# Optimization experiments

Measured on AMD Instinct MI355X. Metric: run time of the kernel, lower is better.

## Reference

```python
import jax, jax.numpy as jnp
import numpy as np

B, C, D = 16384, 512, 512
EXT = 2
H = C * EXT
TAU = 1.0          # temperature_train
STEP = 0.05        # langevin_step_size
NOISE = 0.1        # langevin_noise
STEPS = 32         # langevin_steps


def setup_inputs() -> dict:
    key = jax.random.key(0)
    ks = jax.random.split(key, 8)
    s_in = 1.0 / np.sqrt(D)
    s_h = 1.0 / np.sqrt(H)
    return {
        'x': jax.random.normal(ks[0], (B, D), jnp.float32),
        'vanilla_components': jnp.abs(jax.random.normal(ks[1], (C, D), jnp.float32) * 0.1),
        'e_sp': jax.random.normal(ks[2], (C * D,), jnp.float32) * 0.1,
        'W1e': jax.random.normal(ks[3], (D, H), jnp.float32) * s_in,
        'b1e': jnp.zeros((H,), jnp.float32),
        'W2e': jax.random.normal(ks[4], (H, C), jnp.float32) * s_h,
        'b2e': jnp.zeros((C,), jnp.float32),
        'W1r': jax.random.normal(ks[5], (D, H), jnp.float32) * s_in,
        'b1r': jnp.zeros((H,), jnp.float32),
        'W2r': jax.random.normal(ks[6], (H, C), jnp.float32) * s_h,
        'b2r': jnp.zeros((C,), jnp.float32),
    }


def _langevin_gate(e, key):
    """Langevin MCMC on latent u with quadratic energy E(u)=0.5||u||^2 + <e,u>.
    Returns selection probability sigmoid(-u/tau)."""
    def step(u, k):
        grad = u + e  # dE/du
        u = u - STEP * grad + NOISE * jax.random.normal(k, u.shape, u.dtype)
        return u, None
    u, _ = jax.lax.scan(step, jnp.zeros_like(e), jax.random.split(key, STEPS))
    return jax.nn.sigmoid(-u / TAU)


def reference(x, vanilla_components, e_sp, W1e, b1e, W2e, b2e, W1r, b1r, W2r, b2r):
    k1, k2 = jax.random.split(jax.random.key(42))
    # non-negative components
    comps = jnp.abs(vanilla_components)  # [C, D]
    # fixed energy-based sparsity mask over component entries
    p_sp = _langevin_gate(e_sp, k1).reshape(C, D)
    comps = comps * p_sp
    # dynamic per-sample component selection energies via MLP
    h = jax.nn.relu(x @ W1e + b1e)          # [B, H]
    e_dyn = h @ W2e + b2e                   # [B, C]
    gate = _langevin_gate(e_dyn, k2)        # [B, C] soft gates (train mode)
    hr = jax.nn.relu(x @ W1r + b1r)         # [B, H]
    conc = (hr @ W2r + b2r) * gate          # [B, C]
    # aggregate: (concentration * components).sum over components -> [B, D]
    return conc @ comps
```

## Files before the change

### kernel.cpp

```cpp
#include <hip/hip_runtime.h>
#include <hip/hip_bf16.h>
#include <stdint.h>

#define Bn 16384
#define Cn 512
#define Dn 512
#define Hn 1024

#define A32 0.80628851f

typedef __attribute__((ext_vector_type(8))) short bf16x8;
typedef __attribute__((ext_vector_type(4))) float f32x4;
typedef __attribute__((ext_vector_type(2))) float f32x2;

__device__ __forceinline__ ushort f2bf(float f) {
  uint32_t u = __float_as_uint(f);
  return (ushort)((u + 0x7fffu + ((u >> 16) & 1u)) >> 16);
}
__device__ __forceinline__ float b2f(ushort u) {
  return __uint_as_float((uint32_t)u << 16);
}

typedef __attribute__((address_space(3))) uint32_t lds_u32_t;
typedef const __attribute__((address_space(1))) uint32_t glb_u32_t;
__device__ __forceinline__ void gload16(const ushort* g, ushort* l) {
  __builtin_amdgcn_global_load_lds((glb_u32_t*)g, (lds_u32_t*)l, 16, 0, 0);
}

constexpr uint32_t crotl(uint32_t v, int s) {
  return (v << s) | (v >> (32 - s));
}
struct TFOut { uint32_t w0, w1; };
constexpr TFOut ctf(uint32_t k0, uint32_t k1, uint32_t x0, uint32_t x1) {
  const uint32_t ks[3] = {k0, k1, k0 ^ k1 ^ 0x1BD11BDAu};
  const int rot[8] = {13, 15, 26, 6, 17, 29, 16, 24};
  uint32_t a = x0 + k0, b = x1 + k1;
  for (int g = 0; g < 5; ++g) {
    for (int i = 0; i < 4; ++i) {
      int r = rot[(g & 1) * 4 + i];
      a += b; b = crotl(b, r); b ^= a;
    }
    a += ks[(g + 1) % 3];
    b += ks[(g + 2) % 3] + (uint32_t)(g + 1);
  }
  return {a, b};
}
struct KeySched { uint32_t s[64]; uint32_t d[64]; };
constexpr KeySched make_keys() {
  KeySched K{};
  TFOut k1 = ctf(0u, 42u, 0u, 0u);
  TFOut k2 = ctf(0u, 42u, 0u, 1u);
  for (uint32_t t = 0; t < 32; ++t) {
    TFOut ws = ctf(k1.w0, k1.w1, 0u, t);
    K.s[2 * t] = ws.w0; K.s[2 * t + 1] = ws.w1;
    TFOut wd = ctf(k2.w0, k2.w1, 0u, t);
    K.d[2 * t] = wd.w0; K.d[2 * t + 1] = wd.w1;
  }
  return K;
}
__constant__ KeySched KS = make_keys();

__device__ __forceinline__ uint32_t rotl32(uint32_t v, int s) {
  return __builtin_rotateleft32(v, (uint32_t)s);
}
__device__ __forceinline__ uint32_t tf_xor(uint32_t K0, uint32_t K1,
                                           uint32_t KX, uint32_t j) {
  uint32_t a = K0, b = K1 + j;
#define TR(r) { a += b; b = rotl32(b, (r)); b ^= a; }
  TR(13) TR(15) TR(26) TR(6)   a += K1; b += KX + 1u;
  TR(17) TR(29) TR(16) TR(24)  a += KX; b += K0 + 2u;
  TR(13) TR(15) TR(26) TR(6)   a += K0; b += K1 + 3u;
  TR(17) TR(29) TR(16) TR(24)  a += K1; b += KX + 4u;
  TR(13) TR(15) TR(26) TR(6)   a += KX; b += K0 + 5u;
#undef TR
  return a ^ b;
}

__device__ __forceinline__ float bits_to_normal(uint32_t bits) {
  float f = __uint_as_float((bits >> 9) | 0x3f800000u) - 1.0f;
  float x = f * 2.0f - 0x1.fffffep-1f;
  float w = -__logf(1.0f - x * x);
  float p;
  if (w < 5.0f) {
    w -= 2.5f;
    p =            2.81022636e-08f;
    p = fmaf(p, w, 3.43273939e-07f);
    p = fmaf(p, w, -3.5233877e-06f);
    p = fmaf(p, w, -4.39150654e-06f);
    p = fmaf(p, w, 0.00021858087f);
    p = fmaf(p, w, -0.00125372503f);
    p = fmaf(p, w, -0.00417768164f);
    p = fmaf(p, w, 0.246640727f);
    p = fmaf(p, w, 1.50140941f);
  } else {
    w = sqrtf(w) - 3.0f;
    p =            -0.000200214257f;
    p = fmaf(p, w, 0.000100950558f);
    p = fmaf(p, w, 0.00134934322f);
    p = fmaf(p, w, -0.00367342844f);
    p = fmaf(p, w, 0.00573950773f);
    p = fmaf(p, w, -0.0076224613f);
    p = fmaf(p, w, 0.00943887047f);
    p = fmaf(p, w, 1.00167406f);
    p = fmaf(p, w, 2.83297682f);
  }
  return 0x1.6a09e6p+0f * (p * x);
}

__device__ __forceinline__ void z_block(ushort* __restrict__ Z, uint32_t zidx) {
  const uint32_t j0 = (zidx * 256u + threadIdx.x) * 2u;
  const uint32_t j1 = j0 + 1u;
  float z0 = 0.0f, z1 = 0.0f;
#pragma unroll 4
  for (int t = 0; t < 32; ++t) {
    const uint32_t K0 = KS.d[2 * t], K1 = KS.d[2 * t + 1];
    const uint32_t KX = K0 ^ K1 ^ 0x1BD11BDAu;
    uint32_t a0 = K0, b0 = K1 + j0;
    uint32_t a1 = K0, b1 = K1 + j1;
#define R2(r)                                                  \
    a0 += b0; a1 += b1;                                        \
    b0 = rotl32(b0, (r)); b1 = rotl32(b1, (r));                \
    b0 ^= a0; b1 ^= a1;
#define I2(p, q) a0 += (p); a1 += (p); b0 += (q); b1 += (q);
    R2(13) R2(15) R2(26) R2(6)  I2(K1, KX + 1u)
    R2(17) R2(29) R2(16) R2(24) I2(KX, K0 + 2u)
    R2(13) R2(15) R2(26) R2(6)  I2(K0, K1 + 3u)
    R2(17) R2(29) R2(16) R2(24) I2(K1, KX + 4u)
    R2(13) R2(15) R2(26) R2(6)  I2(KX, K0 + 5u)
#undef R2
#undef I2
    uint32_t s0 = a0 ^ b0, s1 = a1 ^ b1;
    float f0 = __uint_as_float((s0 >> 9) | 0x3f800000u) - 1.0f;
    float f1 = __uint_as_float((s1 >> 9) | 0x3f800000u) - 1.0f;
    float x0 = f0 * 2.0f - 0x1.fffffep-1f;
    float x1 = f1 * 2.0f - 0x1.fffffep-1f;
    float w0 = fminf(-__logf(fmaf(-x0, x0, 1.0f)), 5.0f) - 2.5f;
    float w1 = fminf(-__logf(fmaf(-x1, x1, 1.0f)), 5.0f) - 2.5f;
    f32x2 X = {x0, x1}, W = {w0, w1};
    f32x2 P = {2.81022636e-08f, 2.81022636e-08f};
    P = __builtin_elementwise_fma(P, W, (f32x2){3.43273939e-07f, 3.43273939e-07f});
    P = __builtin_elementwise_fma(P, W, (f32x2){-3.5233877e-06f, -3.5233877e-06f});
    P = __builtin_elementwise_fma(P, W, (f32x2){-4.39150654e-06f, -4.39150654e-06f});
    P = __builtin_elementwise_fma(P, W, (f32x2){0.00021858087f, 0.00021858087f});
    P = __builtin_elementwise_fma(P, W, (f32x2){-0.00125372503f, -0.00125372503f});
    P = __builtin_elementwise_fma(P, W, (f32x2){-0.00417768164f, -0.00417768164f});
    P = __builtin_elementwise_fma(P, W, (f32x2){0.246640727f, 0.246640727f});
    P = __builtin_elementwise_fma(P, W, (f32x2){1.50140941f, 1.50140941f});
    f32x2 Q = (P * X) * (f32x2){0.14142135f, 0.14142135f};
    z0 = fmaf(0.95f, z0, Q.x);
    z1 = fmaf(0.95f, z1, Q.y);
  }
  *(ushort2*)(Z + j0) = make_ushort2(f2bf(z0), f2bf(z1));
}

__device__ __forceinline__ void transpose_tile(
    const float* __restrict__ in, ushort* __restrict__ out,
    int N, int K, int tIdx, float T[32][33]) {
  const int ntn = N / 32;
  const int tk = tIdx / ntn, tn = tIdx % ntn;
  const int tx = threadIdx.x & 31, ty = threadIdx.x >> 5;
  const int k0 = tk * 32, n0 = tn * 32;
#pragma unroll
  for (int r = 0; r < 32; r += 8)
    T[ty + r][tx] = in[(size_t)(k0 + ty + r) * N + n0 + tx];
  __syncthreads();
#pragma unroll
  for (int r = 0; r < 32; r += 8)
    out[(size_t)(n0 + ty + r) * K + k0 + tx] = f2bf(T[tx][ty + r]);
}

__device__ __forceinline__ void smask_block(
    const float* __restrict__ vc, const float* __restrict__ e_sp,
    ushort* __restrict__ compsT, int g) {
  uint32_t jj = (uint32_t)g * 256 + threadIdx.x;
  uint32_t c = jj & (Cn - 1), d = jj >> 9;
  uint32_t ridx = c * Dn + d;
  float e = e_sp[ridx];
  float u = 0.0f;
#pragma unroll 4
  for (int t = 0; t < 32; ++t) {
    const uint32_t K0 = KS.s[2 * t], K1 = KS.s[2 * t + 1];
    uint32_t s = tf_xor(K0, K1, K0 ^ K1 ^ 0x1BD11BDAu, ridx);
    float n = bits_to_normal(s);
    u = (u - 0.05f * (u + e)) + 0.1f * n;
  }
  float gt = 1.0f / (1.0f + __expf(u));
  compsT[jj] = f2bf(fabsf(vc[ridx]) * gt);
}

__global__ __launch_bounds__(256) void k_prep_z(
    const float* __restrict__ x, ushort* __restrict__ x_bf,
    const float* __restrict__ W1e, ushort* __restrict__ W1eT,
    const float* __restrict__ W2e, ushort* __restrict__ W2eT,
    const float* __restrict__ W1r, ushort* __restrict__ W1rT,
    const float* __restrict__ W2r, ushort* __restrict__ W2rT,
    const float* __restrict__ vc, const float* __restrict__ e_sp,
    ushort* __restrict__ compsT, ushort* __restrict__ Zd) {
  __shared__ float T[32][33];
  const int pos = blockIdx.x;
  if ((pos % 5) == 4) {
    z_block(Zd, (uint32_t)(pos / 5));
    return;
  }
  const int p = (pos / 5) * 4 + (pos % 5);
  if (p < 8192) {
    int i = (p * 256 + threadIdx.x) * 4;
    float4 v = *(const float4*)(x + i);
    *(ushort4*)(x_bf + i) =
        make_ushort4(f2bf(v.x), f2bf(v.y), f2bf(v.z), f2bf(v.w));
  } else if (p < 8704) {
    transpose_tile(W1e, W1eT, Hn, Dn, p - 8192, T);
  } else if (p < 9216) {
    transpose_tile(W2e, W2eT, Cn, Hn, p - 8704, T);
  } else if (p < 9728) {
    transpose_tile(W1r, W1rT, Hn, Dn, p - 9216, T);
  } else if (p < 10240) {
    transpose_tile(W2r, W2rT, Cn, Hn, p - 9728, T);
  } else {
    smask_block(vc, e_sp, compsT, p - 10240);
  }
}

__device__ __forceinline__ void stage4(
    const ushort* ga0, const ushort* ga1,
    const ushort* gb0, const ushort* gb1,
    int k, ushort* As, ushort* Bs, int wo) {
  gload16(ga0 + k, As + wo);
  gload16(ga1 + k, As + 2048 + wo);
  gload16(gb0 + k, Bs + wo);
  gload16(gb1 + k, Bs + 2048 + wo);
}

__device__ __forceinline__ void mfma16(
    const ushort* Ac, const ushort* Bc,
    int wm, int wn, int l15, int rc, f32x4 acc[4][4]) {
  bf16x8 af[4], bfr[4];
#pragma unroll
  for (int i = 0; i < 4; ++i) {
    af[i]  = *(const bf16x8*)&Ac[(wm + i * 16 + l15) * 32 + rc];
    bfr[i] = *(const bf16x8*)&Bc[(wn + i * 16 + l15) * 32 + rc];
  }
#pragma unroll
  for (int i = 0; i < 4; ++i)
#pragma unroll
    for (int j = 0; j < 4; ++j)
      acc[i][j] = __builtin_amdgcn_mfma_f32_16x16x32_bf16(af[i], bfr[j],
                                                          acc[i][j], 0, 0, 0);
}

__device__ __forceinline__ void gemm_core(
    const ushort* __restrict__ A, const ushort* __restrict__ WT,
    int m0, int n0, int LD, int K,
    ushort* __restrict__ As0, ushort* __restrict__ Bs0,
    ushort* __restrict__ As1, ushort* __restrict__ Bs1,
    f32x4 acc[4][4]) {
  const int t = threadIdx.x;
  const int wave = t >> 6, lane = t & 63;
  const int row = t >> 2;
  const int col8 = ((t & 3) << 3) ^ (((t >> 3) & 3) << 3);
  const int wm = (wave >> 1) << 6, wn = (wave & 1) << 6;
  const int quad = lane >> 4, l15 = lane & 15;
  const int rc = (quad << 3) ^ (((l15 >> 1) & 3) << 3);
  const int wo = wave * 512;

  const ushort* ga0 = A  + (size_t)(m0 + row) * LD + col8;
  const ushort* ga1 = A  + (size_t)(m0 + 64 + row) * LD + col8;
  const ushort* gb0 = WT + (size_t)(n0 + row) * LD + col8;
  const ushort* gb1 = WT + (size_t)(n0 + 64 + row) * LD + col8;

  stage4(ga0, ga1, gb0, gb1, 0, As0, Bs0, wo);

  for (int k0 = 0; k0 < K; k0 += 64) {
    stage4(ga0, ga1, gb0, gb1, k0 + 32, As1, Bs1, wo);
    asm volatile("s_waitcnt vmcnt(4)" ::: "memory");
    __builtin_amdgcn_sched_barrier(0);
    __builtin_amdgcn_s_barrier();
    mfma16(As0, Bs0, wm, wn, l15, rc, acc);
    __builtin_amdgcn_s_barrier();
    if (k0 + 64 < K) {
      stage4(ga0, ga1, gb0, gb1, k0 + 64, As0, Bs0, wo);
      asm volatile("s_waitcnt vmcnt(4)" ::: "memory");
    } else {
      asm volatile("s_waitcnt vmcnt(0)" ::: "memory");
    }
    __builtin_amdgcn_sched_barrier(0);
    __builtin_amdgcn_s_barrier();
    mfma16(As1, Bs1, wm, wn, l15, rc, acc);
    __builtin_amdgcn_s_barrier();
  }
}

__device__ __forceinline__ void gemm_tile_bf(
    const ushort* __restrict__ A, const ushort* __restrict__ WT,
    const float* __restrict__ bias, ushort* __restrict__ Out, int g,
    ushort* As0, ushort* Bs0, ushort* As1, ushort* Bs1) {
  const int n0 = (g & 7) * 128, m0 = (g >> 3) * 128;
  const int t = threadIdx.x;
  const int wave = t >> 6, lane = t & 63;
  const int wm = (wave >> 1) << 6, wn = (wave & 1) << 6;
  const int quad = lane >> 4, l15 = lane & 15;
  f32x4 acc[4][4] = {};
  gemm_core(A, WT, m0, n0, Dn, Dn, As0, Bs0, As1, Bs1, acc);
#pragma unroll
  for (int i = 0; i < 4; ++i)
#pragma unroll
    for (int j = 0; j < 4; ++j) {
      const int col = n0 + wn + j * 16 + l15;
      const float bv = bias[col];
#pragma unroll
      for (int r = 0; r < 4; ++r) {
        const int row = m0 + wm + i * 16 + quad * 4 + r;
        Out[(size_t)row * Hn + col] = f2bf(fmaxf(acc[i][j][r] + bv, 0.0f));
      }
    }
}

__global__ __launch_bounds__(256) void k_g13_z(
    const ushort* __restrict__ x_bf,
    const ushort* __restrict__ W1eT, const float* __restrict__ b1e,
    ushort* __restrict__ h,
    const ushort* __restrict__ W1rT, const float* __restrict__ b1r,
    ushort* __restrict__ hr, ushort* __restrict__ Zd) {
  __shared__ ushort As0[4096];
  __shared__ ushort Bs0[4096];
  __shared__ ushort As1[4096];
  __shared__ ushort Bs1[4096];
  const int pos = blockIdx.x;
  if (pos % 3) {
    z_block(Zd, 2816u + (uint32_t)(pos / 3) * 2u + (uint32_t)(pos % 3) - 1u);
    return;
  }
  const int gg = pos / 3;
  const int g = gg >> 1;
  if (gg & 1)
    gemm_tile_bf(x_bf, W1rT, b1r, hr, g, As0, Bs0, As1, Bs1);
  else
    gemm_tile_bf(x_bf, W1eT, b1e, h, g, As0, Bs0, As1, Bs1);
}

__device__ __forceinline__ void gemm_tile_f32out(
    const ushort* __restrict__ A, const ushort* __restrict__ WT,
    const float* __restrict__ bias, float* __restrict__ Out,
    int m0, int n0, ushort* As0, ushort* Bs0, ushort* As1, ushort* Bs1) {
  const int t = threadIdx.x;
  const int wave = t >> 6, lane = t & 63;
  const int wm = (wave >> 1) << 6, wn = (wave & 1) << 6;
  const int quad = lane >> 4, l15 = lane & 15;
  f32x4 acc[4][4] = {};
  gemm_core(A, WT, m0, n0, Hn, Hn, As0, Bs0, As1, Bs1, acc);
#pragma unroll
  for (int i = 0; i < 4; ++i)
#pragma unroll
    for (int j = 0; j < 4; ++j) {
      const int col = n0 + wn + j * 16 + l15;
      const float bv = bias[col];
#pragma unroll
      for (int r = 0; r < 4; ++r) {
        const int row = m0 + wm + i * 16 + quad * 4 + r;
        Out[(size_t)row * Cn + col] = acc[i][j][r] + bv;
      }
    }
}

__global__ __launch_bounds__(256) void k_e_z(
    const ushort* __restrict__ h, const ushort* __restrict__ W2eT,
    const float* __restrict__ b2e, float* __restrict__ e_out,
    ushort* __restrict__ Zd) {
  __shared__ ushort As0[4096];
  __shared__ ushort Bs0[4096];
  __shared__ ushort As1[4096];
  __shared__ ushort Bs1[4096];
  const int pos = blockIdx.x;
  if ((pos % 10) == 0) {
    const int tg = pos / 10;
    gemm_tile_f32out(h, W2eT, b2e, e_out, (tg >> 2) * 128, (tg & 3) * 128,
                     As0, Bs0, As1, Bs1);
  } else {
    z_block(Zd, 6912u + (uint32_t)(pos / 10) * 9u + (uint32_t)(pos % 10) - 1u);
  }
}

__global__ __launch_bounds__(256) void k_r_z(
    const ushort* __restrict__ hr, const ushort* __restrict__ W2rT,
    const float* __restrict__ b2r, float* __restrict__ cr_out,
    ushort* __restrict__ Zd) {
  __shared__ ushort As0[4096];
  __shared__ ushort Bs0[4096];
  __shared__ ushort As1[4096];
  __shared__ ushort Bs1[4096];
  const int pos = blockIdx.x;
  if (pos >= 5120) {
    z_block(Zd, 16128u + (uint32_t)(pos - 5120));
    return;
  }
  if ((pos % 10) == 0) {
    const int tg = pos / 10;
    gemm_tile_f32out(hr, W2rT, b2r, cr_out, (tg >> 2) * 128, (tg & 3) * 128,
                     As0, Bs0, As1, Bs1);
  } else {
    z_block(Zd, 11520u + (uint32_t)(pos / 10) * 9u + (uint32_t)(pos % 10) - 1u);
  }
}

__global__ __launch_bounds__(256) void k_gate(
    const float* __restrict__ e, const float* __restrict__ cr,
    ushort* __restrict__ Z) {
  const size_t i = ((size_t)blockIdx.x * 256u + threadIdx.x) * 8u;
  uint4 zv = *(const uint4*)(Z + i);
  ushort zs[8];
  *(uint4*)zs = zv;
  float ee[8], cc[8];
  *(float4*)(ee)     = *(const float4*)(e + i);
  *(float4*)(ee + 4) = *(const float4*)(e + i + 4);
  *(float4*)(cc)     = *(const float4*)(cr + i);
  *(float4*)(cc + 4) = *(const float4*)(cr + i + 4);
  ushort os[8];
#pragma unroll
  for (int k = 0; k < 8; ++k) {
    float z = b2f(zs[k]);
    float g = 1.0f / (1.0f + __expf(z - A32 * ee[k]));
    os[k] = f2bf(cc[k] * g);
  }
  *(uint4*)(Z + i) = *(uint4*)os;
}

__global__ __launch_bounds__(256) void k_gemm_out(
    const ushort* __restrict__ A, const ushort* __restrict__ WT,
    float* __restrict__ Out) {
  __shared__ ushort As0[4096];
  __shared__ ushort Bs0[4096];
  __shared__ ushort As1[4096];
  __shared__ ushort Bs1[4096];
  const int t = threadIdx.x;
  const int m0 = blockIdx.y * 128, n0 = blockIdx.x * 128;
  const int wave = t >> 6, lane = t & 63;
  const int wm = (wave >> 1) << 6, wn = (wave & 1) << 6;
  const int quad = lane >> 4, l15 = lane & 15;
  f32x4 acc[4][4] = {};
  gemm_core(A, WT, m0, n0, Cn, Cn, As0, Bs0, As1, Bs1, acc);
#pragma unroll
  for (int i = 0; i < 4; ++i)
#pragma unroll
    for (int j = 0; j < 4; ++j) {
      const int col = n0 + wn + j * 16 + l15;
#pragma unroll
      for (int r = 0; r < 4; ++r) {
        const int row = m0 + wm + i * 16 + quad * 4 + r;
        Out[(size_t)row * Dn + col] = acc[i][j][r];
      }
    }
}

extern "C" void kernel_launch(void* const* d_in, const int* in_sizes, int n_in,
                              void* d_out, int out_size, void* d_ws, size_t ws_size,
                              hipStream_t stream) {
  const float* x    = (const float*)d_in[0];
  const float* vc   = (const float*)d_in[1];
  const float* e_sp = (const float*)d_in[2];
  const float* W1e  = (const float*)d_in[3];
  const float* b1e  = (const float*)d_in[4];
  const float* W2e  = (const float*)d_in[5];
  const float* b2e  = (const float*)d_in[6];
  const float* W1r  = (const float*)d_in[7];
  const float* b1r  = (const float*)d_in[8];
  const float* W2r  = (const float*)d_in[9];
  const float* b2r  = (const float*)d_in[10];
  float* out = (float*)d_out;

  char* ws = (char*)d_ws;
  ushort* W1eT   = (ushort*)(ws + (1u << 12));
  ushort* W2eT   = (ushort*)(ws + (1u << 12) + (1u << 20));
  ushort* W1rT   = (ushort*)(ws + (1u << 12) + (2u << 20));
  ushort* W2rT   = (ushort*)(ws + (1u << 12) + (3u << 20));
  ushort* compsT = (ushort*)(ws + (1u << 12) + (4u << 20));
  ushort* Zdyn   = (ushort*)(ws + (8u << 20));
  ushort* h_bf   = (ushort*)(ws + (24u << 20));
  ushort* hr_bf  = (ushort*)(ws + (56u << 20));
  float*  cr_f32 = (float*)(ws + (24u << 20));
  ushort* x_bf   = (ushort*)d_out;
  float*  e_f32  = (float*)d_out;

  k_prep_z<<<14080, 256, 0, stream>>>(x, x_bf, W1e, W1eT, W2e, W2eT,
                                      W1r, W1rT, W2r, W2rT, vc, e_sp, compsT,
                                      Zdyn);
  k_g13_z<<<6144, 256, 0, stream>>>(x_bf, W1eT, b1e, h_bf, W1rT, b1r, hr_bf,
                                    Zdyn);
  k_e_z<<<5120, 256, 0, stream>>>(h_bf, W2eT, b2e, e_f32, Zdyn);
  k_r_z<<<5376, 256, 0, stream>>>(hr_bf, W2rT, b2r, cr_f32, Zdyn);
  k_gate<<<4096, 256, 0, stream>>>(e_f32, cr_f32, Zdyn);
  k_gemm_out<<<dim3(Dn / 128, Bn / 128), 256, 0, stream>>>(Zdyn, compsT, out);
}
```

Measured before the change: 777.5 us.

## Shrink MLP GEMM tiles to 64x64 with single-buffer LDS and higher occupancy

Replaces the 128x128 double-buffered GEMM core used by the three MLP GEMMs with a 64x64 tile, single-buffered LDS loop that synchronizes every 32-wide K step. Launch bounds request 8 blocks per CU, and grid interleaving with the Z-noise generation blocks is remapped to match the new tile counts. The output GEMM keeps the original pipelined 128x128 core, now inlined. Smaller tiles raise occupancy and interleaving granularity, but they lower data reuse per loaded byte and lose the load/compute overlap of the double buffer.

Result: slower. 844.6 us (+8.6%).

```diff
diff --git a/kernel.cpp b/kernel.cpp
--- a/kernel.cpp
+++ b/kernel.cpp
@@ -188,7 +188,7 @@
   compsT[jj] = f2bf(fabsf(vc[ridx]) * gt);
 }
 
-__global__ __launch_bounds__(256) void k_prep_z(
+__global__ __launch_bounds__(256, 8) void k_prep_z(
     const float* __restrict__ x, ushort* __restrict__ x_bf,
     const float* __restrict__ W1e, ushort* __restrict__ W1eT,
     const float* __restrict__ W2e, ushort* __restrict__ W2eT,
@@ -221,184 +221,143 @@
   }
 }
 
-__device__ __forceinline__ void stage4(
-    const ushort* ga0, const ushort* ga1,
-    const ushort* gb0, const ushort* gb1,
-    int k, ushort* As, ushort* Bs, int wo) {
-  gload16(ga0 + k, As + wo);
-  gload16(ga1 + k, As + 2048 + wo);
-  gload16(gb0 + k, Bs + wo);
-  gload16(gb1 + k, Bs + 2048 + wo);
-}
-
-__device__ __forceinline__ void mfma16(
-    const ushort* Ac, const ushort* Bc,
-    int wm, int wn, int l15, int rc, f32x4 acc[4][4]) {
-  bf16x8 af[4], bfr[4];
-#pragma unroll
-  for (int i = 0; i < 4; ++i) {
-    af[i]  = *(const bf16x8*)&Ac[(wm + i * 16 + l15) * 32 + rc];
-    bfr[i] = *(const bf16x8*)&Bc[(wn + i * 16 + l15) * 32 + rc];
-  }
-#pragma unroll
-  for (int i = 0; i < 4; ++i)
-#pragma unroll
-    for (int j = 0; j < 4; ++j)
-      acc[i][j] = __builtin_amdgcn_mfma_f32_16x16x32_bf16(af[i], bfr[j],
-                                                          acc[i][j], 0, 0, 0);
-}
-
-__device__ __forceinline__ void gemm_core(
+__device__ __forceinline__ void gemm_core64(
     const ushort* __restrict__ A, const ushort* __restrict__ WT,
     int m0, int n0, int LD, int K,
-    ushort* __restrict__ As0, ushort* __restrict__ Bs0,
-    ushort* __restrict__ As1, ushort* __restrict__ Bs1,
-    f32x4 acc[4][4]) {
+    ushort* __restrict__ AsL, ushort* __restrict__ BsL,
+    f32x4 acc[2][2]) {
   const int t = threadIdx.x;
   const int wave = t >> 6, lane = t & 63;
   const int row = t >> 2;
   const int col8 = ((t & 3) << 3) ^ (((t >> 3) & 3) << 3);
-  const int wm = (wave >> 1) << 6, wn = (wave & 1) << 6;
+  const int wr = (wave >> 1) << 5, wc = (wave & 1) << 5;
   const int quad = lane >> 4, l15 = lane & 15;
   const int rc = (quad << 3) ^ (((l15 >> 1) & 3) << 3);
-  const int wo = wave * 512;
-
-  const ushort* ga0 = A  + (size_t)(m0 + row) * LD + col8;
-  const ushort* ga1 = A  + (size_t)(m0 + 64 + row) * LD + col8;
-  const ushort* gb0 = WT + (size_t)(n0 + row) * LD + col8;
-  const ushort* gb1 = WT + (size_t)(n0 + 64 + row) * LD + col8;
-
-  stage4(ga0, ga1, gb0, gb1, 0, As0, Bs0, wo);
-
-  for (int k0 = 0; k0 < K; k0 += 64) {
-    stage4(ga0, ga1, gb0, gb1, k0 + 32, As1, Bs1, wo);
-    asm volatile("s_waitcnt vmcnt(4)" ::: "memory");
-    __builtin_amdgcn_sched_barrier(0);
-    __builtin_amdgcn_s_barrier();
-    mfma16(As0, Bs0, wm, wn, l15, rc, acc);
-    __builtin_amdgcn_s_barrier();
-    if (k0 + 64 < K) {
-      stage4(ga0, ga1, gb0, gb1, k0 + 64, As0, Bs0, wo);
-      asm volatile("s_waitcnt vmcnt(4)" ::: "memory");
-    } else {
-      asm volatile("s_waitcnt vmcnt(0)" ::: "memory");
+
+  const ushort* ga = A  + (size_t)(m0 + row) * LD + col8;
+  const ushort* gb = WT + (size_t)(n0 + row) * LD + col8;
+  ushort* la = AsL + wave * 512;
+  ushort* lb = BsL + wave * 512;
+
+  for (int k0 = 0; k0 < K; k0 += 32) {
+    gload16(ga + k0, la);
+    gload16(gb + k0, lb);
+    __syncthreads();
+    bf16x8 af[2], bfr[2];
+#pragma unroll
+    for (int i = 0; i < 2; ++i) {
+      af[i]  = *(const bf16x8*)&AsL[(wr + i * 16 + l15) * 32 + rc];
+      bfr[i] = *(const bf16x8*)&BsL[(wc + i * 16 + l15) * 32 + rc];
     }
-    __builtin_amdgcn_sched_barrier(0);
-    __builtin_amdgcn_s_barrier();
-    mfma16(As1, Bs1, wm, wn, l15, rc, acc);
-    __builtin_amdgcn_s_barrier();
-  }
-}
-
-__device__ __forceinline__ void gemm_tile_bf(
+#pragma unroll
+    for (int i = 0; i < 2; ++i)
+#pragma unroll
+      for (int j = 0; j < 2; ++j)
+        acc[i][j] = __builtin_amdgcn_mfma_f32_16x16x32_bf16(af[i], bfr[j],
+                                                            acc[i][j], 0, 0, 0);
+    __syncthreads();
+  }
+}
+
+__device__ __forceinline__ void gemm_tile_bf64(
     const ushort* __restrict__ A, const ushort* __restrict__ WT,
-    const float* __restrict__ bias, ushort* __restrict__ Out, int g,
-    ushort* As0, ushort* Bs0, ushort* As1, ushort* Bs1) {
-  const int n0 = (g & 7) * 128, m0 = (g >> 3) * 128;
+    const float* __restrict__ bias, ushort* __restrict__ Out,
+    int m0, int n0, ushort* AsL, ushort* BsL) {
   const int t = threadIdx.x;
   const int wave = t >> 6, lane = t & 63;
-  const int wm = (wave >> 1) << 6, wn = (wave & 1) << 6;
+  const int wr = (wave >> 1) << 5, wc = (wave & 1) << 5;
   const int quad = lane >> 4, l15 = lane & 15;
-  f32x4 acc[4][4] = {};
-  gemm_core(A, WT, m0, n0, Dn, Dn, As0, Bs0, As1, Bs1, acc);
-#pragma unroll
-  for (int i = 0; i < 4; ++i)
-#pragma unroll
-    for (int j = 0; j < 4; ++j) {
-      const int col = n0 + wn + j * 16 + l15;
+  f32x4 acc[2][2] = {};
+  gemm_core64(A, WT, m0, n0, Dn, Dn, AsL, BsL, acc);
+#pragma unroll
+  for (int i = 0; i < 2; ++i)
+#pragma unroll
+    for (int j = 0; j < 2; ++j) {
+      const int col = n0 + wc + j * 16 + l15;
       const float bv = bias[col];
 #pragma unroll
       for (int r = 0; r < 4; ++r) {
-        const int row = m0 + wm + i * 16 + quad * 4 + r;
+        const int row = m0 + wr + i * 16 + quad * 4 + r;
         Out[(size_t)row * Hn + col] = f2bf(fmaxf(acc[i][j][r] + bv, 0.0f));
       }
     }
 }
 
-__global__ __launch_bounds__(256) void k_g13_z(
+__global__ __launch_bounds__(256, 8) void k_g13_z(
     const ushort* __restrict__ x_bf,
     const ushort* __restrict__ W1eT, const float* __restrict__ b1e,
     ushort* __restrict__ h,
     const ushort* __restrict__ W1rT, const float* __restrict__ b1r,
     ushort* __restrict__ hr, ushort* __restrict__ Zd) {
-  __shared__ ushort As0[4096];
-  __shared__ ushort Bs0[4096];
-  __shared__ ushort As1[4096];
-  __shared__ ushort Bs1[4096];
+  __shared__ ushort AsL[2048];
+  __shared__ ushort BsL[2048];
   const int pos = blockIdx.x;
-  if (pos % 3) {
-    z_block(Zd, 2816u + (uint32_t)(pos / 3) * 2u + (uint32_t)(pos % 3) - 1u);
+  if ((pos % 3) == 2) {
+    z_block(Zd, 2816u + (uint32_t)(pos / 3));
     return;
   }
-  const int gg = pos / 3;
+  const int gg = (pos / 3) * 2 + (pos % 3);
   const int g = gg >> 1;
+  const int m0 = (g >> 4) * 64, n0 = (g & 15) * 64;
   if (gg & 1)
-    gemm_tile_bf(x_bf, W1rT, b1r, hr, g, As0, Bs0, As1, Bs1);
+    gemm_tile_bf64(x_bf, W1rT, b1r, hr, m0, n0, AsL, BsL);
   else
-    gemm_tile_bf(x_bf, W1eT, b1e, h, g, As0, Bs0, As1, Bs1);
-}
-
-__device__ __forceinline__ void gemm_tile_f32out(
+    gemm_tile_bf64(x_bf, W1eT, b1e, h, m0, n0, AsL, BsL);
+}
+
+__device__ __forceinline__ void gemm_tile_f32out64(
     const ushort* __restrict__ A, const ushort* __restrict__ WT,
     const float* __restrict__ bias, float* __restrict__ Out,
-    int m0, int n0, ushort* As0, ushort* Bs0, ushort* As1, ushort* Bs1) {
+    int m0, int n0, ushort* AsL, ushort* BsL) {
   const int t = threadIdx.x;
   const int wave = t >> 6, lane = t & 63;
-  const int wm = (wave >> 1) << 6, wn = (wave & 1) << 6;
+  const int wr = (wave >> 1) << 5, wc = (wave & 1) << 5;
   const int quad = lane >> 4, l15 = lane & 15;
-  f32x4 acc[4][4] = {};
-  gemm_core(A, WT, m0, n0, Hn, Hn, As0, Bs0, As1, Bs1, acc);
-#pragma unroll
-  for (int i = 0; i < 4; ++i)
-#pragma unroll
-    for (int j = 0; j < 4; ++j) {
-      const int col = n0 + wn + j * 16 + l15;
+  f32x4 acc[2][2] = {};
+  gemm_core64(A, WT, m0, n0, Hn, Hn, AsL, BsL, acc);
+#pragma unroll
+  for (int i = 0; i < 2; ++i)
+#pragma unroll
+    for (int j = 0; j < 2; ++j) {
+      const int col = n0 + wc + j * 16 + l15;
       const float bv = bias[col];
 #pragma unroll
       for (int r = 0; r < 4; ++r) {
-        const int row = m0 + wm + i * 16 + quad * 4 + r;
+        const int row = m0 + wr + i * 16 + quad * 4 + r;
         Out[(size_t)row * Cn + col] = acc[i][j][r] + bv;
       }
     }
 }
 
-__global__ __launch_bounds__(256) void k_e_z(
+__global__ __launch_bounds__(256, 8) void k_e_z(
     const ushort* __restrict__ h, const ushort* __restrict__ W2eT,
     const float* __restrict__ b2e, float* __restrict__ e_out,
     ushort* __restrict__ Zd) {
-  __shared__ ushort As0[4096];
-  __shared__ ushort Bs0[4096];
-  __shared__ ushort As1[4096];
-  __shared__ ushort Bs1[4096];
+  __shared__ ushort AsL[2048];
+  __shared__ ushort BsL[2048];
   const int pos = blockIdx.x;
-  if ((pos % 10) == 0) {
-    const int tg = pos / 10;
-    gemm_tile_f32out(h, W2eT, b2e, e_out, (tg >> 2) * 128, (tg & 3) * 128,
-                     As0, Bs0, As1, Bs1);
+  if ((pos % 13) < 4) {
+    const int tg = (pos / 13) * 4 + (pos % 13);
+    gemm_tile_f32out64(h, W2eT, b2e, e_out, (tg >> 3) * 64, (tg & 7) * 64,
+                       AsL, BsL);
   } else {
-    z_block(Zd, 6912u + (uint32_t)(pos / 10) * 9u + (uint32_t)(pos % 10) - 1u);
-  }
-}
-
-__global__ __launch_bounds__(256) void k_r_z(
+    z_block(Zd, 6912u + (uint32_t)((pos / 13) * 9 + (pos % 13) - 4));
+  }
+}
+
+__global__ __launch_bounds__(256, 8) void k_r_z(
     const ushort* __restrict__ hr, const ushort* __restrict__ W2rT,
     const float* __restrict__ b2r, float* __restrict__ cr_out,
     ushort* __restrict__ Zd) {
-  __shared__ ushort As0[4096];
-  __shared__ ushort Bs0[4096];
-  __shared__ ushort As1[4096];
-  __shared__ ushort Bs1[4096];
+  __shared__ ushort AsL[2048];
+  __shared__ ushort BsL[2048];
   const int pos = blockIdx.x;
-  if (pos >= 5120) {
-    z_block(Zd, 16128u + (uint32_t)(pos - 5120));
-    return;
-  }
-  if ((pos % 10) == 0) {
-    const int tg = pos / 10;
-    gemm_tile_f32out(hr, W2rT, b2r, cr_out, (tg >> 2) * 128, (tg & 3) * 128,
-                     As0, Bs0, As1, Bs1);
+  if ((pos % 27) < 8) {
+    const int tg = (pos / 27) * 8 + (pos % 27);
+    gemm_tile_f32out64(hr, W2rT, b2r, cr_out, (tg >> 3) * 64, (tg & 7) * 64,
+                       AsL, BsL);
   } else {
-    z_block(Zd, 11520u + (uint32_t)(pos / 10) * 9u + (uint32_t)(pos % 10) - 1u);
+    z_block(Zd, 11520u + (uint32_t)((pos / 27) * 19 + (pos % 27) - 8));
   }
 }
 
@@ -424,6 +383,33 @@
   *(uint4*)(Z + i) = *(uint4*)os;
 }
 
+__device__ __forceinline__ void stage4(
+    const ushort* ga0, const ushort* ga1,
+    const ushort* gb0, const ushort* gb1,
+    int k, ushort* As, ushort* Bs, int wo) {
+  gload16(ga0 + k, As + wo);
+  gload16(ga1 + k, As + 2048 + wo);
+  gload16(gb0 + k, Bs + wo);
+  gload16(gb1 + k, Bs + 2048 + wo);
+}
+
+__device__ __forceinline__ void mfma16(
+    const ushort* Ac, const ushort* Bc,
+    int wm, int wn, int l15, int rc, f32x4 acc[4][4]) {
+  bf16x8 af[4], bfr[4];
+#pragma unroll
+  for (int i = 0; i < 4; ++i) {
+    af[i]  = *(const bf16x8*)&Ac[(wm + i * 16 + l15) * 32 + rc];
+    bfr[i] = *(const bf16x8*)&Bc[(wn + i * 16 + l15) * 32 + rc];
+  }
+#pragma unroll
+  for (int i = 0; i < 4; ++i)
+#pragma unroll
+    for (int j = 0; j < 4; ++j)
+      acc[i][j] = __builtin_amdgcn_mfma_f32_16x16x32_bf16(af[i], bfr[j],
+                                                          acc[i][j], 0, 0, 0);
+}
+
 __global__ __launch_bounds__(256) void k_gemm_out(
     const ushort* __restrict__ A, const ushort* __restrict__ WT,
     float* __restrict__ Out) {
@@ -434,10 +420,38 @@
   const int t = threadIdx.x;
   const int m0 = blockIdx.y * 128, n0 = blockIdx.x * 128;
   const int wave = t >> 6, lane = t & 63;
+  const int row = t >> 2;
+  const int col8 = ((t & 3) << 3) ^ (((t >> 3) & 3) << 3);
   const int wm = (wave >> 1) << 6, wn = (wave & 1) << 6;
   const int quad = lane >> 4, l15 = lane & 15;
+  const int rc = (quad << 3) ^ (((l15 >> 1) & 3) << 3);
+  const int wo = wave * 512;
+
+  const ushort* ga0 = A  + (size_t)(m0 + row) * Cn + col8;
+  const ushort* ga1 = A  + (size_t)(m0 + 64 + row) * Cn + col8;
+  const ushort* gb0 = WT + (size_t)(n0 + row) * Cn + col8;
+  const ushort* gb1 = WT + (size_t)(n0 + 64 + row) * Cn + col8;
+
   f32x4 acc[4][4] = {};
-  gemm_core(A, WT, m0, n0, Cn, Cn, As0, Bs0, As1, Bs1, acc);
+  stage4(ga0, ga1, gb0, gb1, 0, As0, Bs0, wo);
+  for (int k0 = 0; k0 < Cn; k0 += 64) {
+    stage4(ga0, ga1, gb0, gb1, k0 + 32, As1, Bs1, wo);
+    asm volatile("s_waitcnt vmcnt(4)" ::: "memory");
+    __builtin_amdgcn_sched_barrier(0);
+    __builtin_amdgcn_s_barrier();
+    mfma16(As0, Bs0, wm, wn, l15, rc, acc);
+    __builtin_amdgcn_s_barrier();
+    if (k0 + 64 < Cn) {
+      stage4(ga0, ga1, gb0, gb1, k0 + 64, As0, Bs0, wo);
+      asm volatile("s_waitcnt vmcnt(4)" ::: "memory");
+    } else {
+      asm volatile("s_waitcnt vmcnt(0)" ::: "memory");
+    }
+    __builtin_amdgcn_sched_barrier(0);
+    __builtin_amdgcn_s_barrier();
+    mfma16(As1, Bs1, wm, wn, l15, rc, acc);
+    __builtin_amdgcn_s_barrier();
+  }
 #pragma unroll
   for (int i = 0; i < 4; ++i)
 #pragma unroll
@@ -445,8 +459,8 @@
       const int col = n0 + wn + j * 16 + l15;
 #pragma unroll
       for (int r = 0; r < 4; ++r) {
-        const int row = m0 + wm + i * 16 + quad * 4 + r;
-        Out[(size_t)row * Dn + col] = acc[i][j][r];
+        const int row2 = m0 + wm + i * 16 + quad * 4 + r;
+        Out[(size_t)row2 * Dn + col] = acc[i][j][r];
       }
     }
 }
@@ -483,10 +497,10 @@
   k_prep_z<<<14080, 256, 0, stream>>>(x, x_bf, W1e, W1eT, W2e, W2eT,
                                       W1r, W1rT, W2r, W2rT, vc, e_sp, compsT,
                                       Zdyn);
-  k_g13_z<<<6144, 256, 0, stream>>>(x_bf, W1eT, b1e, h_bf, W1rT, b1r, hr_bf,
-                                    Zdyn);
-  k_e_z<<<5120, 256, 0, stream>>>(h_bf, W2eT, b2e, e_f32, Zdyn);
-  k_r_z<<<5376, 256, 0, stream>>>(hr_bf, W2rT, b2r, cr_f32, Zdyn);
+  k_g13_z<<<12288, 256, 0, stream>>>(x_bf, W1eT, b1e, h_bf, W1rT, b1r, hr_bf,
+                                     Zdyn);
+  k_e_z<<<6656, 256, 0, stream>>>(h_bf, W2eT, b2e, e_f32, Zdyn);
+  k_r_z<<<6912, 256, 0, stream>>>(hr_bf, W2rT, b2r, cr_f32, Zdyn);
   k_gate<<<4096, 256, 0, stream>>>(e_f32, cr_f32, Zdyn);
   k_gemm_out<<<dim3(Dn / 128, Bn / 128), 256, 0, stream>>>(Zdyn, compsT, out);
 }
```

## Fuse Langevin noise generation into first-layer GEMM k-loop with 512-thread blocks

Applied to the files above, without the earlier changes.

Replaces the interleaved grid of separate GEMM blocks and RNG-only blocks with 512-thread blocks that each compute a 128x128 GEMM tile and, inside every k-iteration, also run two Langevin noise steps for their own slice of Z. The aim is to hide the VALU-heavy Threefry/erfinv work under MFMA and memory latency inside the same wave. The GEMM becomes single-buffered with a 32-wide k-step and two syncthreads per iteration, which loses the previous double-buffered prefetch. It also raises register pressure under launch_bounds(512,6).

Measured after the change: 771.3 us. No clear change (-0.8%).

```diff
diff --git a/kernel.cpp b/kernel.cpp
--- a/kernel.cpp
+++ b/kernel.cpp
@@ -107,49 +107,52 @@
   return 0x1.6a09e6p+0f * (p * x);
 }
 
+__device__ __forceinline__ void z_step(int t, uint32_t j0, uint32_t j1,
+                                       float& z0, float& z1) {
+  const uint32_t K0 = KS.d[2 * t], K1 = KS.d[2 * t + 1];
+  const uint32_t KX = K0 ^ K1 ^ 0x1BD11BDAu;
+  uint32_t a0 = K0, b0 = K1 + j0;
+  uint32_t a1 = K0, b1 = K1 + j1;
+#define R2(r)                                                  \
+  a0 += b0; a1 += b1;                                          \
+  b0 = rotl32(b0, (r)); b1 = rotl32(b1, (r));                  \
+  b0 ^= a0; b1 ^= a1;
+#define I2(p, q) a0 += (p); a1 += (p); b0 += (q); b1 += (q);
+  R2(13) R2(15) R2(26) R2(6)  I2(K1, KX + 1u)
+  R2(17) R2(29) R2(16) R2(24) I2(KX, K0 + 2u)
+  R2(13) R2(15) R2(26) R2(6)  I2(K0, K1 + 3u)
+  R2(17) R2(29) R2(16) R2(24) I2(K1, KX + 4u)
+  R2(13) R2(15) R2(26) R2(6)  I2(KX, K0 + 5u)
+#undef R2
+#undef I2
+  uint32_t s0 = a0 ^ b0, s1 = a1 ^ b1;
+  float f0 = __uint_as_float((s0 >> 9) | 0x3f800000u) - 1.0f;
+  float f1 = __uint_as_float((s1 >> 9) | 0x3f800000u) - 1.0f;
+  float x0 = f0 * 2.0f - 0x1.fffffep-1f;
+  float x1 = f1 * 2.0f - 0x1.fffffep-1f;
+  float w0 = fminf(-__logf(fmaf(-x0, x0, 1.0f)), 5.0f) - 2.5f;
+  float w1 = fminf(-__logf(fmaf(-x1, x1, 1.0f)), 5.0f) - 2.5f;
+  f32x2 X = {x0, x1}, W = {w0, w1};
+  f32x2 P = {2.81022636e-08f, 2.81022636e-08f};
+  P = __builtin_elementwise_fma(P, W, (f32x2){3.43273939e-07f, 3.43273939e-07f});
+  P = __builtin_elementwise_fma(P, W, (f32x2){-3.5233877e-06f, -3.5233877e-06f});
+  P = __builtin_elementwise_fma(P, W, (f32x2){-4.39150654e-06f, -4.39150654e-06f});
+  P = __builtin_elementwise_fma(P, W, (f32x2){0.00021858087f, 0.00021858087f});
+  P = __builtin_elementwise_fma(P, W, (f32x2){-0.00125372503f, -0.00125372503f});
+  P = __builtin_elementwise_fma(P, W, (f32x2){-0.00417768164f, -0.00417768164f});
+  P = __builtin_elementwise_fma(P, W, (f32x2){0.246640727f, 0.246640727f});
+  P = __builtin_elementwise_fma(P, W, (f32x2){1.50140941f, 1.50140941f});
+  f32x2 Q = (P * X) * (f32x2){0.14142135f, 0.14142135f};
+  z0 = fmaf(0.95f, z0, Q.x);
+  z1 = fmaf(0.95f, z1, Q.y);
+}
+
 __device__ __forceinline__ void z_block(ushort* __restrict__ Z, uint32_t zidx) {
   const uint32_t j0 = (zidx * 256u + threadIdx.x) * 2u;
   const uint32_t j1 = j0 + 1u;
   float z0 = 0.0f, z1 = 0.0f;
 #pragma unroll 4
-  for (int t = 0; t < 32; ++t) {
-    const uint32_t K0 = KS.d[2 * t], K1 = KS.d[2 * t + 1];
-    const uint32_t KX = K0 ^ K1 ^ 0x1BD11BDAu;
-    uint32_t a0 = K0, b0 = K1 + j0;
-    uint32_t a1 = K0, b1 = K1 + j1;
-#define R2(r)                                                  \
-    a0 += b0; a1 += b1;                                        \
-    b0 = rotl32(b0, (r)); b1 = rotl32(b1, (r));                \
-    b0 ^= a0; b1 ^= a1;
-#define I2(p, q) a0 += (p); a1 += (p); b0 += (q); b1 += (q);
-    R2(13) R2(15) R2(26) R2(6)  I2(K1, KX + 1u)
-    R2(17) R2(29) R2(16) R2(24) I2(KX, K0 + 2u)
-    R2(13) R2(15) R2(26) R2(6)  I2(K0, K1 + 3u)
-    R2(17) R2(29) R2(16) R2(24) I2(K1, KX + 4u)
-    R2(13) R2(15) R2(26) R2(6)  I2(KX, K0 + 5u)
-#undef R2
-#undef I2
-    uint32_t s0 = a0 ^ b0, s1 = a1 ^ b1;
-    float f0 = __uint_as_float((s0 >> 9) | 0x3f800000u) - 1.0f;
-    float f1 = __uint_as_float((s1 >> 9) | 0x3f800000u) - 1.0f;
-    float x0 = f0 * 2.0f - 0x1.fffffep-1f;
-    float x1 = f1 * 2.0f - 0x1.fffffep-1f;
-    float w0 = fminf(-__logf(fmaf(-x0, x0, 1.0f)), 5.0f) - 2.5f;
-    float w1 = fminf(-__logf(fmaf(-x1, x1, 1.0f)), 5.0f) - 2.5f;
-    f32x2 X = {x0, x1}, W = {w0, w1};
-    f32x2 P = {2.81022636e-08f, 2.81022636e-08f};
-    P = __builtin_elementwise_fma(P, W, (f32x2){3.43273939e-07f, 3.43273939e-07f});
-    P = __builtin_elementwise_fma(P, W, (f32x2){-3.5233877e-06f, -3.5233877e-06f});
-    P = __builtin_elementwise_fma(P, W, (f32x2){-4.39150654e-06f, -4.39150654e-06f});
-    P = __builtin_elementwise_fma(P, W, (f32x2){0.00021858087f, 0.00021858087f});
-    P = __builtin_elementwise_fma(P, W, (f32x2){-0.00125372503f, -0.00125372503f});
-    P = __builtin_elementwise_fma(P, W, (f32x2){-0.00417768164f, -0.00417768164f});
-    P = __builtin_elementwise_fma(P, W, (f32x2){0.246640727f, 0.246640727f});
-    P = __builtin_elementwise_fma(P, W, (f32x2){1.50140941f, 1.50140941f});
-    f32x2 Q = (P * X) * (f32x2){0.14142135f, 0.14142135f};
-    z0 = fmaf(0.95f, z0, Q.x);
-    z1 = fmaf(0.95f, z1, Q.y);
-  }
+  for (int t = 0; t < 32; ++t) z_step(t, j0, j1, z0, z1);
   *(ushort2*)(Z + j0) = make_ushort2(f2bf(z0), f2bf(z1));
 }
 
@@ -219,6 +222,87 @@
   } else {
     smask_block(vc, e_sp, compsT, p - 10240);
   }
+}
+
+template <int KIT, int ZS>
+__device__ __forceinline__ void gemm_z_fused(
+    const ushort* __restrict__ A, const ushort* __restrict__ WT,
+    int m0, int n0, int LD,
+    ushort* __restrict__ AsL, ushort* __restrict__ BsL,
+    f32x4 acc[4][2], uint32_t j0, uint32_t j1, float& z0, float& z1) {
+  const int t = threadIdx.x;
+  const int wave = t >> 6, lane = t & 63;
+  const int row = t >> 2;
+  const int col8 = ((t & 3) << 3) ^ (((t >> 3) & 3) << 3);
+  const int wm = (wave >> 2) << 6, wn = (wave & 3) << 5;
+  const int l15 = lane & 15, quad = lane >> 4;
+  const int rc = (quad << 3) ^ (((l15 >> 1) & 3) << 3);
+
+  const ushort* ga = A  + (size_t)(m0 + row) * LD + col8;
+  const ushort* gb = WT + (size_t)(n0 + row) * LD + col8;
+  ushort* la = AsL + wave * 512;
+  ushort* lb = BsL + wave * 512;
+
+  for (int it = 0; it < KIT; ++it) {
+    gload16(ga + it * 32, la);
+    gload16(gb + it * 32, lb);
+    __syncthreads();
+    bf16x8 af[4], bfr[2];
+#pragma unroll
+    for (int i = 0; i < 4; ++i)
+      af[i] = *(const bf16x8*)&AsL[(wm + i * 16 + l15) * 32 + rc];
+#pragma unroll
+    for (int j = 0; j < 2; ++j)
+      bfr[j] = *(const bf16x8*)&BsL[(wn + j * 16 + l15) * 32 + rc];
+#pragma unroll
+    for (int i = 0; i < 4; ++i)
+#pragma unroll
+      for (int j = 0; j < 2; ++j)
+        acc[i][j] = __builtin_amdgcn_mfma_f32_16x16x32_bf16(af[i], bfr[j],
+                                                            acc[i][j], 0, 0, 0);
+#pragma unroll
+    for (int s = 0; s < ZS; ++s)
+      z_step(it * ZS + s, j0, j1, z0, z1);
+    __syncthreads();
+  }
+}
+
+__global__ __launch_bounds__(512, 6) void k_g13_z(
+    const ushort* __restrict__ x_bf,
+    const ushort* __restrict__ W1eT, const float* __restrict__ b1e,
+    ushort* __restrict__ h,
+    const ushort* __restrict__ W1rT, const float* __restrict__ b1r,
+    ushort* __restrict__ hr, ushort* __restrict__ Zd) {
+  __shared__ ushort AsL[4096];
+  __shared__ ushort BsL[4096];
+  const int pos = blockIdx.x;
+  const uint32_t j0 = 1441792u + (uint32_t)pos * 1024u +
+                      (uint32_t)threadIdx.x * 2u;
+  const uint32_t j1 = j0 + 1u;
+  float z0 = 0.0f, z1 = 0.0f;
+  const int tg = pos >> 1;
+  const int m0 = (tg >> 3) * 128, n0 = (tg & 7) * 128;
+  const ushort* WTp = (pos & 1) ? W1rT : W1eT;
+  const float*  bp  = (pos & 1) ? b1r  : b1e;
+  ushort*       Op  = (pos & 1) ? hr   : h;
+  f32x4 acc[4][2] = {};
+  gemm_z_fused<16, 2>(x_bf, WTp, m0, n0, Dn, AsL, BsL, acc, j0, j1, z0, z1);
+  *(ushort2*)(Zd + j0) = make_ushort2(f2bf(z0), f2bf(z1));
+  const int wave = threadIdx.x >> 6, lane = threadIdx.x & 63;
+  const int wm = (wave >> 2) << 6, wn = (wave & 3) << 5;
+  const int quad = lane >> 4, l15 = lane & 15;
+#pragma unroll
+  for (int i = 0; i < 4; ++i)
+#pragma unroll
+    for (int j = 0; j < 2; ++j) {
+      const int col = n0 + wn + j * 16 + l15;
+      const float bv = bp[col];
+#pragma unroll
+      for (int r = 0; r < 4; ++r) {
+        const int row = m0 + wm + i * 16 + quad * 4 + r;
+        Op[(size_t)row * Hn + col] = f2bf(fmaxf(acc[i][j][r] + bv, 0.0f));
+      }
+    }
 }
 
 __device__ __forceinline__ void stage4(
@@ -290,54 +374,6 @@
   }
 }
 
-__device__ __forceinline__ void gemm_tile_bf(
-    const ushort* __restrict__ A, const ushort* __restrict__ WT,
-    const float* __restrict__ bias, ushort* __restrict__ Out, int g,
-    ushort* As0, ushort* Bs0, ushort* As1, ushort* Bs1) {
-  const int n0 = (g & 7) * 128, m0 = (g >> 3) * 128;
-  const int t = threadIdx.x;
-  const int wave = t >> 6, lane = t & 63;
-  const int wm = (wave >> 1) << 6, wn = (wave & 1) << 6;
-  const int quad = lane >> 4, l15 = lane & 15;
-  f32x4 acc[4][4] = {};
-  gemm_core(A, WT, m0, n0, Dn, Dn, As0, Bs0, As1, Bs1, acc);
-#pragma unroll
-  for (int i = 0; i < 4; ++i)
-#pragma unroll
-    for (int j = 0; j < 4; ++j) {
-      const int col = n0 + wn + j * 16 + l15;
-      const float bv = bias[col];
-#pragma unroll
-      for (int r = 0; r < 4; ++r) {
-        const int row = m0 + wm + i * 16 + quad * 4 + r;
-        Out[(size_t)row * Hn + col] = f2bf(fmaxf(acc[i][j][r] + bv, 0.0f));
-      }
-    }
-}
-
-__global__ __launch_bounds__(256) void k_g13_z(
-    const ushort* __restrict__ x_bf,
-    const ushort* __restrict__ W1eT, const float* __restrict__ b1e,
-    ushort* __restrict__ h,
-    const ushort* __restrict__ W1rT, const float* __restrict__ b1r,
-    ushort* __restrict__ hr, ushort* __restrict__ Zd) {
-  __shared__ ushort As0[4096];
-  __shared__ ushort Bs0[4096];
-  __shared__ ushort As1[4096];
-  __shared__ ushort Bs1[4096];
-  const int pos = blockIdx.x;
-  if (pos % 3) {
-    z_block(Zd, 2816u + (uint32_t)(pos / 3) * 2u + (uint32_t)(pos % 3) - 1u);
-    return;
-  }
-  const int gg = pos / 3;
-  const int g = gg >> 1;
-  if (gg & 1)
-    gemm_tile_bf(x_bf, W1rT, b1r, hr, g, As0, Bs0, As1, Bs1);
-  else
-    gemm_tile_bf(x_bf, W1eT, b1e, h, g, As0, Bs0, As1, Bs1);
-}
-
 __device__ __forceinline__ void gemm_tile_f32out(
     const ushort* __restrict__ A, const ushort* __restrict__ WT,
     const float* __restrict__ bias, float* __restrict__ Out,
@@ -445,8 +481,8 @@
       const int col = n0 + wn + j * 16 + l15;
 #pragma unroll
       for (int r = 0; r < 4; ++r) {
-        const int row = m0 + wm + i * 16 + quad * 4 + r;
-        Out[(size_t)row * Dn + col] = acc[i][j][r];
+        const int row2 = m0 + wm + i * 16 + quad * 4 + r;
+        Out[(size_t)row2 * Dn + col] = acc[i][j][r];
       }
     }
 }
@@ -483,7 +519,7 @@
   k_prep_z<<<14080, 256, 0, stream>>>(x, x_bf, W1e, W1eT, W2e, W2eT,
                                       W1r, W1rT, W2r, W2rT, vc, e_sp, compsT,
                                       Zdyn);
-  k_g13_z<<<6144, 256, 0, stream>>>(x_bf, W1eT, b1e, h_bf, W1rT, b1r, hr_bf,
+  k_g13_z<<<2048, 512, 0, stream>>>(x_bf, W1eT, b1e, h_bf, W1rT, b1r, hr_bf,
                                     Zdyn);
   k_e_z<<<5120, 256, 0, stream>>>(h_bf, W2eT, b2e, e_f32, Zdyn);
   k_r_z<<<5376, 256, 0, stream>>>(hr_bf, W2rT, b2r, cr_f32, Zdyn);
```
